# Optimization experiments

Measured on AMD Instinct MI355X. Metric: run time of the kernel, lower is better.

Reference implementation:

```python
import jax, jax.numpy as jnp
import numpy as np

ROWS, COLS = 64, 64  # map size[:2]


def setup_inputs() -> dict:
    key = jax.random.key(0)
    k1, k2 = jax.random.split(key)
    B, D = 128, 256
    x = jax.random.normal(k1, (B, D), dtype=jnp.float32)
    weights = jax.random.normal(k2, (ROWS, COLS, D), dtype=jnp.float32)
    return {"x": x, "weights": weights}


def reference(x, weights):
    """Som.forward in training mode.

    distances : [B, rows*cols] euclidean distance (squared_dist = sqrt(sum((a-b)^2)))
    bmus      : [B, 2] (row, col) of argmin neuron
    diffs     : [B, rows, cols, D] elementwise x - weight (stored for the update step)
    """
    B, D = x.shape
    w_flat = weights.reshape(-1, D)  # [M, D], M = rows*cols
    # Euclidean distance via the GEMM expansion: |a-b|^2 = |a|^2 + |b|^2 - 2 a.b
    x_sq = jnp.sum(x * x, axis=-1, keepdims=True)          # [B, 1]
    w_sq = jnp.sum(w_flat * w_flat, axis=-1)               # [M]
    d2 = x_sq + w_sq[None, :] - 2.0 * (x @ w_flat.T)       # [B, M]
    distances = jnp.sqrt(jnp.maximum(d2, 0.0))
    min_idx = jnp.argmin(distances, axis=-1)               # [B]
    bmus = jnp.stack([min_idx // COLS, min_idx % COLS], axis=1)  # [B, 2]
    # elementwise diff tensor materialized by the training forward
    diffs = x[:, None, None, :] - weights[None, :, :, :]   # [B, rows, cols, D]
    return bmus, diffs
```

## Files before the change

kernel.cpp:

```cpp
#include <hip/hip_runtime.h>

#define BATCH 128
#define SOM_ROWS 64
#define SOM_COLS 64
#define M (SOM_ROWS * SOM_COLS)
#define D 256
#define DV (D / 4)

__global__ void som_diffs_dist(const float* __restrict__ x,
                               const float* __restrict__ w,
                               float* __restrict__ diffs,
                               float* __restrict__ d2ws) {
  const int lane = threadIdx.x & 63;
  const int wave_in_block = threadIdx.x >> 6;
  const int waves_per_block = blockDim.x >> 6;
  const long gwave = (long)blockIdx.x * waves_per_block + wave_in_block;
  const long nwaves = (long)gridDim.x * waves_per_block;

  const float4* __restrict__ x4 = (const float4*)x;
  const float4* __restrict__ w4 = (const float4*)w;
  float4* __restrict__ o4 = (float4*)diffs;

  const long nrows = (long)BATCH * M;
  for (long r = gwave; r < nrows; r += nwaves) {
    const int b = (int)(r >> 12);
    const int m = (int)(r & (M - 1));
    const float4 xv = x4[b * DV + lane];
    const float4 wv = w4[m * DV + lane];
    float4 dv;
    dv.x = xv.x - wv.x;
    dv.y = xv.y - wv.y;
    dv.z = xv.z - wv.z;
    dv.w = xv.w - wv.w;
    o4[r * DV + lane] = dv;
    float s = dv.x * dv.x + dv.y * dv.y + dv.z * dv.z + dv.w * dv.w;
#pragma unroll
    for (int off = 32; off; off >>= 1) s += __shfl_xor(s, off, 64);
    if (lane == 0) d2ws[r] = s;
  }
}

__global__ void som_argmin(const float* __restrict__ d2ws,
                           float* __restrict__ out) {
  __shared__ float sval[256];
  __shared__ int sidx[256];
  const int b = blockIdx.x;
  const int t = threadIdx.x;
  float best = 3.4e38f;
  int bidx = 0x7fffffff;
  for (int m = t; m < M; m += 256) {
    const float v = d2ws[b * M + m];
    if (v < best) {
      best = v;
      bidx = m;
    }
  }
  sval[t] = best;
  sidx[t] = bidx;
  __syncthreads();
  for (int s = 128; s; s >>= 1) {
    if (t < s) {
      const float v2 = sval[t + s];
      const int i2 = sidx[t + s];
      if (v2 < sval[t] || (v2 == sval[t] && i2 < sidx[t])) {
        sval[t] = v2;
        sidx[t] = i2;
      }
    }
    __syncthreads();
  }
  if (t == 0) {
    out[2 * b] = (float)(sidx[0] / SOM_COLS);
    out[2 * b + 1] = (float)(sidx[0] % SOM_COLS);
  }
}

extern "C" void kernel_launch(void* const* d_in, const int* in_sizes, int n_in,
                              void* d_out, int out_size, void* d_ws,
                              size_t ws_size, hipStream_t stream) {
  const float* x = (const float*)d_in[0];
  const float* w = (const float*)d_in[1];
  float* out = (float*)d_out;
  float* bmus = out;
  float* diffs = out + 2 * BATCH;
  float* d2ws = (float*)d_ws;

  som_diffs_dist<<<2048, 256, 0, stream>>>(x, w, diffs, d2ws);
  som_argmin<<<BATCH, 256, 0, stream>>>(d2ws, bmus);
}
```

Baseline: 572.5 us.

## Split distance/argmin from diff write and use nontemporal stores

Removes the per-row distance workspace: a separate kernel recomputes squared distances per batch row from x held in LDS and w, then does the argmin directly. The diff-writing kernel now keeps one w row in registers per wave, loops over batches with four stores in flight, and uses nontemporal stores for the 512 MB output. The intent is to cut the workspace traffic and the strided per-row loop overhead, at the cost of reading w again in the argmin kernel.

```diff
diff --git a/kernel.cpp b/kernel.cpp
--- a/kernel.cpp
+++ b/kernel.cpp
@@ -7,61 +7,88 @@
 #define D 256
 #define DV (D / 4)
 
-__global__ void som_diffs_dist(const float* __restrict__ x,
-                               const float* __restrict__ w,
-                               float* __restrict__ diffs,
-                               float* __restrict__ d2ws) {
+typedef float f32x4 __attribute__((ext_vector_type(4)));
+
+__global__ void __launch_bounds__(256) som_diffs(const float* __restrict__ x,
+                                                 const float* __restrict__ w,
+                                                 float* __restrict__ diffs) {
   const int lane = threadIdx.x & 63;
-  const int wave_in_block = threadIdx.x >> 6;
-  const int waves_per_block = blockDim.x >> 6;
-  const long gwave = (long)blockIdx.x * waves_per_block + wave_in_block;
-  const long nwaves = (long)gridDim.x * waves_per_block;
+  const int wib = threadIdx.x >> 6;
+  const int gwave = blockIdx.x * (blockDim.x >> 6) + wib;
+  const int m = gwave & (M - 1);
+  const int b0 = gwave >> 12;
 
-  const float4* __restrict__ x4 = (const float4*)x;
-  const float4* __restrict__ w4 = (const float4*)w;
-  float4* __restrict__ o4 = (float4*)diffs;
+  const f32x4* __restrict__ x4 = (const f32x4*)x;
+  const f32x4* __restrict__ w4 = (const f32x4*)w;
+  f32x4* __restrict__ o4 = (f32x4*)diffs;
 
-  const long nrows = (long)BATCH * M;
-  for (long r = gwave; r < nrows; r += nwaves) {
-    const int b = (int)(r >> 12);
-    const int m = (int)(r & (M - 1));
-    const float4 xv = x4[b * DV + lane];
-    const float4 wv = w4[m * DV + lane];
-    float4 dv;
-    dv.x = xv.x - wv.x;
-    dv.y = xv.y - wv.y;
-    dv.z = xv.z - wv.z;
-    dv.w = xv.w - wv.w;
-    o4[r * DV + lane] = dv;
-    float s = dv.x * dv.x + dv.y * dv.y + dv.z * dv.z + dv.w * dv.w;
-#pragma unroll
-    for (int off = 32; off; off >>= 1) s += __shfl_xor(s, off, 64);
-    if (lane == 0) d2ws[r] = s;
+  const f32x4 wv = w4[m * DV + lane];
+
+  for (int b = b0; b < BATCH; b += 8) {
+    f32x4 x0 = x4[(b + 0) * DV + lane];
+    f32x4 x1 = x4[(b + 2) * DV + lane];
+    f32x4 x2 = x4[(b + 4) * DV + lane];
+    f32x4 x3 = x4[(b + 6) * DV + lane];
+    f32x4 d0 = x0 - wv;
+    f32x4 d1 = x1 - wv;
+    f32x4 d2 = x2 - wv;
+    f32x4 d3 = x3 - wv;
+    __builtin_nontemporal_store(d0, &o4[((long)(b + 0) * M + m) * DV + lane]);
+    __builtin_nontemporal_store(d1, &o4[((long)(b + 2) * M + m) * DV + lane]);
+    __builtin_nontemporal_store(d2, &o4[((long)(b + 4) * M + m) * DV + lane]);
+    __builtin_nontemporal_store(d3, &o4[((long)(b + 6) * M + m) * DV + lane]);
   }
 }
 
-__global__ void som_argmin(const float* __restrict__ d2ws,
-                           float* __restrict__ out) {
-  __shared__ float sval[256];
-  __shared__ int sidx[256];
+__global__ void __launch_bounds__(512) som_dist_argmin(
+    const float* __restrict__ x, const float* __restrict__ w,
+    float* __restrict__ out) {
+  __shared__ f32x4 xs[DV];
+  __shared__ float sval[512];
+  __shared__ int sidx[512];
   const int b = blockIdx.x;
   const int t = threadIdx.x;
+  const int lane = t & 63;
+  const int wid = t >> 6;
+  const int g = lane >> 4;
+  const int c = lane & 15;
+
+  const f32x4* __restrict__ x4 = (const f32x4*)x;
+  const f32x4* __restrict__ w4 = (const f32x4*)w;
+
+  if (t < DV) xs[t] = x4[b * DV + t];
+  __syncthreads();
+
   float best = 3.4e38f;
   int bidx = 0x7fffffff;
-  for (int m = t; m < M; m += 256) {
-    const float v = d2ws[b * M + m];
-    if (v < best) {
-      best = v;
+
+  for (int step = 0; step < 128; ++step) {
+    const int m = (wid << 9) + (step << 2) + g;
+    float s = 0.f;
+#pragma unroll
+    for (int j = 0; j < 4; ++j) {
+      const f32x4 wv = w4[(long)m * DV + (j << 4) + c];
+      const f32x4 xv = xs[(j << 4) + c];
+      const f32x4 df = xv - wv;
+      s += df.x * df.x + df.y * df.y + df.z * df.z + df.w * df.w;
+    }
+    s += __shfl_xor(s, 1, 64);
+    s += __shfl_xor(s, 2, 64);
+    s += __shfl_xor(s, 4, 64);
+    s += __shfl_xor(s, 8, 64);
+    if (s < best) {
+      best = s;
       bidx = m;
     }
   }
+
   sval[t] = best;
   sidx[t] = bidx;
   __syncthreads();
-  for (int s = 128; s; s >>= 1) {
-    if (t < s) {
-      const float v2 = sval[t + s];
-      const int i2 = sidx[t + s];
+  for (int sr = 256; sr; sr >>= 1) {
+    if (t < sr) {
+      const float v2 = sval[t + sr];
+      const int i2 = sidx[t + sr];
       if (v2 < sval[t] || (v2 == sval[t] && i2 < sidx[t])) {
         sval[t] = v2;
         sidx[t] = i2;
@@ -70,8 +97,8 @@
     __syncthreads();
   }
   if (t == 0) {
-    out[2 * b] = (float)(sidx[0] / SOM_COLS);
-    out[2 * b + 1] = (float)(sidx[0] % SOM_COLS);
+    out[2 * b] = (float)(sidx[0] >> 6);
+    out[2 * b + 1] = (float)(sidx[0] & 63);
   }
 }
 
@@ -83,8 +110,7 @@
   float* out = (float*)d_out;
   float* bmus = out;
   float* diffs = out + 2 * BATCH;
-  float* d2ws = (float*)d_ws;
 
-  som_diffs_dist<<<2048, 256, 0, stream>>>(x, w, diffs, d2ws);
-  som_argmin<<<BATCH, 256, 0, stream>>>(d2ws, bmus);
+  som_dist_argmin<<<BATCH, 512, 0, stream>>>(x, w, bmus);
+  som_diffs<<<2048, 256, 0, stream>>>(x, w, diffs);
 }
```

Result: slower. 609.8 us (+6.5%).
